# Optimization experiments

Measured on AMD Instinct MI355X. Metric: run time of the kernel, lower is better.

Reference implementation:

```python
import jax, jax.numpy as jnp
import numpy as np

HIDDEN = 1024
HEADS = 16
HEAD_DIM = HIDDEN // HEADS
ROTARY_PCT = 0.25
ROTARY_DIM = int(HEAD_DIM * ROTARY_PCT)  # 16
BASE = 10000.0
SCALE = HEAD_DIM ** -0.5
EPS = 1e-8


def _rotate_half(x):
    h = x.shape[-1] // 2
    return jnp.concatenate([-x[..., h:], x[..., :h]], axis=-1)


def _apply_rope(q, k, position_ids):
    # q, k: [B, H, S, D]; NeoX-style partial rotary on first ROTARY_DIM dims
    inv_freq = 1.0 / (BASE ** (jnp.arange(0, ROTARY_DIM, 2, dtype=jnp.float32) / ROTARY_DIM))
    freqs = position_ids.astype(jnp.float32)[:, None] * inv_freq[None, :]  # [S, rd/2]
    emb = jnp.concatenate([freqs, freqs], axis=-1)  # [S, rd]
    cos = jnp.cos(emb)[None, None, :, :]
    sin = jnp.sin(emb)[None, None, :, :]

    def rot(x):
        x_rot, x_pass = x[..., :ROTARY_DIM], x[..., ROTARY_DIM:]
        x_rot = x_rot * cos + _rotate_half(x_rot) * sin
        return jnp.concatenate([x_rot, x_pass], axis=-1)

    return rot(q), rot(k)


def _ka_scan(attn_weights, value):
    # attn_weights: [B, H, S, S] causal softmax; value: [B, H, S, D]
    # A[0] = V[0]; A[i] = renorm(attn_weights[i, :i]) @ A[:i]
    S = value.shape[2]
    idx = jnp.arange(S)

    def step(a_buf, i):
        w = attn_weights[:, :, i, :]                      # [B, H, S]
        w = jnp.where(idx[None, None, :] < i, w, 0.0)     # strict past only
        w = w / (jnp.sum(w, axis=-1, keepdims=True) + EPS)
        a_i = jnp.einsum('bhs,bhsd->bhd', w, a_buf)
        a_i = jnp.where(i == 0, value[:, :, 0, :], a_i)
        a_buf = jax.lax.dynamic_update_slice(a_buf, a_i[:, :, None, :], (0, 0, i, 0))
        return a_buf, None

    a_buf, _ = jax.lax.scan(step, jnp.zeros_like(value), jnp.arange(S))
    return a_buf


def setup_inputs() -> dict:
    key = jax.random.key(0)
    k1, k2, k3 = jax.random.split(key, 3)
    B, S = 2, 2048
    hidden_states = jax.random.normal(k1, (B, S, HIDDEN), dtype=jnp.float32)
    position_ids = jnp.arange(S, dtype=jnp.int32)
    Wqkv = jax.random.normal(k2, (HIDDEN, 3 * HIDDEN), dtype=jnp.float32) / np.sqrt(HIDDEN)
    bqkv = jnp.zeros((3 * HIDDEN,), dtype=jnp.float32)
    Wd = jax.random.normal(k3, (HIDDEN, HIDDEN), dtype=jnp.float32) / np.sqrt(HIDDEN)
    bd = jnp.zeros((HIDDEN,), dtype=jnp.float32)
    return {"hidden_states": hidden_states, "position_ids": position_ids,
            "Wqkv": Wqkv, "bqkv": bqkv, "Wd": Wd, "bd": bd}


def reference(hidden_states, position_ids, Wqkv, bqkv, Wd, bd):
    B, S, _ = hidden_states.shape
    qkv = hidden_states @ Wqkv + bqkv                       # [B, S, 3*hidden]
    qkv = qkv.reshape(B, S, 3, HEADS, HEAD_DIM).transpose(2, 0, 3, 1, 4)
    query, key, value = qkv[0], qkv[1], qkv[2]              # [B, H, S, D]
    query, key = _apply_rope(query, key, position_ids)

    scores = jnp.einsum('bhqd,bhkd->bhqk', query, key) * SCALE
    causal = jnp.tril(jnp.ones((S, S), dtype=bool))
    scores = jnp.where(causal[None, None], scores, -jnp.inf)
    attn_weights = jax.nn.softmax(scores, axis=-1)          # [B, H, S, S]

    attn_output = _ka_scan(attn_weights, value)             # [B, H, S, D]
    attn_output = attn_output.transpose(0, 2, 1, 3).reshape(B, S, HIDDEN)
    return attn_output @ Wd + bd
```

## Files before the change

### kernel.cpp

```cpp
#include <hip/hip_runtime.h>

#define S_ 2048
#define EPSF 1e-8f
#define SCALEF 0.125f

typedef short bf16x8 __attribute__((ext_vector_type(8)));
typedef float f32x4 __attribute__((ext_vector_type(4)));

__device__ __forceinline__ unsigned short f2bf(float f){
  unsigned int u = __float_as_uint(f);
  u = (u + 0x7fffu + ((u >> 16) & 1u)) >> 16;
  return (unsigned short)u;
}
__device__ __forceinline__ float bf2f(unsigned short h){
  return __uint_as_float(((unsigned int)h) << 16);
}
__device__ __forceinline__ unsigned short f2bf_trunc(float f){
  return (unsigned short)(__float_as_uint(f) >> 16);
}

#define GLD16(g, l) __builtin_amdgcn_global_load_lds( \
    (const __attribute__((address_space(1))) unsigned int*)(g), \
    (__attribute__((address_space(3))) unsigned int*)(l), 16, 0, 0)

__global__ void k_prep(const float* __restrict__ hs, const float* __restrict__ Wqkv,
                       const float* __restrict__ bqkv, const float* __restrict__ Wd,
                       unsigned short* __restrict__ Ab,
                       unsigned short* __restrict__ WT,
                       float* __restrict__ U,
                       float* __restrict__ c_c){
  __shared__ float t[32][33];
  __shared__ float red[4][64];
  __shared__ float vsh[64];
  int bid = blockIdx.x;
  if (bid < 4096){
    int i = (bid * 256 + threadIdx.x) * 4;
    float4 v = *(const float4*)(hs + i);
    ushort4 o; o.x=f2bf(v.x); o.y=f2bf(v.y); o.z=f2bf(v.z); o.w=f2bf(v.w);
    *(ushort4*)(Ab + i) = o;
  } else if (bid < 6144){
    int q = bid - 4096;
    int nt = q & 63, kt = q >> 6;
    int tx = threadIdx.x & 31, ty = threadIdx.x >> 5;
    #pragma unroll
    for (int r = 0; r < 32; r += 8)
      t[ty + r][tx] = Wqkv[(size_t)(kt*32 + ty + r)*3072 + nt*32 + tx];
    __syncthreads();
    #pragma unroll
    for (int r = 0; r < 32; r += 8)
      WT[(size_t)(nt*32 + ty + r)*1024 + kt*32 + tx] = f2bf(t[tx][ty + r]);
  } else if (bid < 6176){
    int bh = bid - 6144; int b = bh >> 4, h = bh & 15;
    int d = threadIdx.x & 63, kc = threadIdx.x >> 6;
    const float* x = hs + (size_t)b * S_ * 1024;
    int col = 2048 + h*64 + d;
    float acc = 0.f;
    #pragma unroll 8
    for (int k = kc*256; k < kc*256 + 256; ++k)
      acc = fmaf(x[k], Wqkv[(size_t)k*3072 + col], acc);
    red[kc][d] = acc;
    __syncthreads();
    if (kc == 0)
      vsh[d] = red[0][d] + red[1][d] + red[2][d] + red[3][d] + bqkv[col];
    __syncthreads();
    for (int n = threadIdx.x; n < 1024; n += 256){
      float a2 = 0.f;
      #pragma unroll 8
      for (int dd = 0; dd < 64; ++dd)
        a2 = fmaf(vsh[dd], Wd[(size_t)(h*64 + dd)*1024 + n], a2);
      U[(size_t)bh*1024 + n] = a2;
    }
  } else {
    int q = bid - 6176;
    float4 z = (float4){0.f,0.f,0.f,0.f};
    *(float4*)(c_c + (size_t)q*1024 + threadIdx.x*4) = z;
  }
}

#define BK 32
__launch_bounds__(256)
__global__ void k_gemm_qk(const unsigned short* __restrict__ Ab,
                          const unsigned short* __restrict__ WT,
                          const float* __restrict__ bqkv,
                          const int* __restrict__ pos_ids,
                          unsigned short* __restrict__ Qb,
                          unsigned short* __restrict__ Kb){
  __shared__ unsigned short At[128*BK];
  __shared__ unsigned short Bt[128*BK];
  const int m0 = blockIdx.y * 128, n0 = blockIdx.x * 128;
  const int w = threadIdx.x >> 6, l = threadIdx.x & 63;
  const int wr = w >> 1, wc = w & 1;
  const int lq = l & 15, lh = l >> 4;
  f32x4 acc[4][4];
  #pragma unroll
  for (int i = 0; i < 4; ++i)
    #pragma unroll
    for (int j = 0; j < 4; ++j) acc[i][j] = (f32x4){0.f,0.f,0.f,0.f};

  const int srow = l >> 2;
  const int scol = (l & 3) * 8;

  for (int kt = 0; kt < 1024; kt += BK){
    GLD16(Ab + (size_t)(m0 + w*32 +      srow)*1024 + kt + scol, &At[(w*32)*BK]);
    GLD16(Ab + (size_t)(m0 + w*32 + 16 + srow)*1024 + kt + scol, &At[(w*32+16)*BK]);
    GLD16(WT + (size_t)(n0 + w*32 +      srow)*1024 + kt + scol, &Bt[(w*32)*BK]);
    GLD16(WT + (size_t)(n0 + w*32 + 16 + srow)*1024 + kt + scol, &Bt[(w*32+16)*BK]);
    __syncthreads();
    bf16x8 af[4], bf[4];
    #pragma unroll
    for (int i = 0; i < 4; ++i)
      af[i] = *(const bf16x8*)&At[(wr*64 + i*16 + lq)*BK + lh*8];
    #pragma unroll
    for (int j = 0; j < 4; ++j)
      bf[j] = *(const bf16x8*)&Bt[(wc*64 + j*16 + lq)*BK + lh*8];
    #pragma unroll
    for (int i = 0; i < 4; ++i)
      #pragma unroll
      for (int j = 0; j < 4; ++j)
        acc[i][j] = __builtin_amdgcn_mfma_f32_16x16x32_bf16(af[i], bf[j], acc[i][j], 0, 0, 0);
    __syncthreads();
  }
  #pragma unroll
  for (int i = 0; i < 4; ++i){
    #pragma unroll
    for (int j = 0; j < 4; ++j){
      #pragma unroll
      for (int r = 0; r < 4; ++r){
        int m = m0 + wr*64 + i*16 + (l>>4)*4 + r;
        int n = n0 + wc*64 + j*16 + (l&15);
        float v = acc[i][j][r] + bqkv[n];
        if (j == 0){
          float partner = __shfl_xor(v, 8);
          int s = m & 2047;
          float pos = (float)pos_ids[s];
          float fr = exp2f(-1.6609640474436813f * (float)(l & 7));
          float th = pos * fr;
          float sn = __sinf(th), cn = __cosf(th);
          v = ((l & 8) == 0) ? (v*cn - partner*sn) : (v*cn + partner*sn);
        }
        int b = m >> 11, s2 = m & 2047;
        int tsel = n >> 10; int nq = n & 1023;
        int h = nq >> 6, d = nq & 63;
        unsigned short* dst = tsel ? Kb : Qb;
        dst[((size_t)(b*16 + h)*S_ + s2)*64 + d] = f2bf(v);
      }
    }
  }
}

#define KST2 66
#define EST 68
__launch_bounds__(256, 4)
__global__ void k_scores(const unsigned short* __restrict__ Qb,
                         const unsigned short* __restrict__ Kb,
                         unsigned short* __restrict__ Eg,
                         float* __restrict__ rinvg){
  __shared__ unsigned short Ks[2][64*KST2];
  __shared__ unsigned short Es[4][16*EST];
  __shared__ float dsh[4][16];
  const int bi = blockIdx.x >> 5, bh = blockIdx.x & 31;
  const unsigned short* Qh = Qb + (size_t)bh * S_ * 64;
  const unsigned short* Kh = Kb + (size_t)bh * S_ * 64;
  const int tid = threadIdx.x, w = tid >> 6, l = tid & 63;
  const int lq = l & 15, lh = l >> 4;
  const unsigned short* qp = Qh + (size_t)(bi*64 + w*16 + lq)*64 + lh*8;
  bf16x8 qf0 = *(const bf16x8*)(qp);
  bf16x8 qf1 = *(const bf16x8*)(qp + 32);
  float dacc[4] = {0.f,0.f,0.f,0.f};
  unsigned short* Etile0 = Eg + ((size_t)bh*528 + (size_t)(bi*(bi+1)/2))*4096;
  const int srow = tid >> 2, sc = (tid & 3)*16;

  {
    const unsigned short* src = Kh + (size_t)srow*64 + sc;
    *(int4*)&Ks[0][srow*KST2 + sc]     = *(const int4*)(src);
    *(int4*)&Ks[0][srow*KST2 + sc + 8] = *(const int4*)(src + 8);
  }
  __syncthreads();

  for (int bj = 0; bj <= bi; ++bj){
    const int cur = bj & 1;
    int4 nk0, nk1;
    if (bj < bi){
      const unsigned short* src = Kh + (size_t)((bj+1)*64 + srow)*64 + sc;
      nk0 = *(const int4*)(src);
      nk1 = *(const int4*)(src + 8);
    }
    unsigned short* Et = Etile0 + (size_t)bj*4096 + w*1024;
    const bool diag = (bj == bi);
    #pragma unroll
    for (int ct = 0; ct < 4; ++ct){
      bf16x8 b0 = *(const bf16x8*)&Ks[cur][(ct*16 + lq)*KST2 + lh*8];
      bf16x8 b1 = *(const bf16x8*)&Ks[cur][(ct*16 + lq)*KST2 + 32 + lh*8];
      f32x4 a = (f32x4){0.f,0.f,0.f,0.f};
      a = __builtin_amdgcn_mfma_f32_16x16x32_bf16(qf0, b0, a, 0, 0, 0);
      a = __builtin_amdgcn_mfma_f32_16x16x32_bf16(qf1, b1, a, 0, 0, 0);
      #pragma unroll
      for (int r = 0; r < 4; ++r){
        float e = __expf(a[r] * SCALEF);
        unsigned short eb = f2bf_trunc(e);
        int rrow = lh*4 + r, col = ct*16 + lq;
        Es[w][rrow*EST + col] = eb;
        float ev = bf2f(eb);
        int grow = w*16 + rrow;
        if (!diag || col < grow) dacc[r] += ev;
        if (diag && col == grow) dsh[w][rrow] = ev;
      }
    }
    #pragma unroll
    for (int it = 0; it < 2; ++it){
      int row = it*8 + (l >> 3), eo = (l & 7)*8;
      *(int4*)(Et + row*64 + eo) = *(const int4*)&Es[w][row*EST + eo];
    }
    if (bj < bi){
      *(int4*)&Ks[cur^1][srow*KST2 + sc]     = nk0;
      *(int4*)&Ks[cur^1][srow*KST2 + sc + 8] = nk1;
    }
    __syncthreads();
  }
  #pragma unroll
  for (int r = 0; r < 4; ++r){
    float d = dacc[r];
    #pragma unroll
    for (int mm = 1; mm < 16; mm <<= 1) d += __shfl_xor(d, mm);
    float dE = dsh[w][lh*4 + r];
    float den = fmaf(EPSF, d + dE, d);
    float rv = 1.0f / den;
    if (lq == 0)
      rinvg[(size_t)bh*S_ + bi*64 + w*16 + lh*4 + r] = rv;
  }
}

__global__ __launch_bounds__(64)
void k_dinv(const unsigned short* __restrict__ Eg,
            const float* __restrict__ rinvg,
            unsigned short* __restrict__ Dg){
  __shared__ float As[64*65];
  const int bh = blockIdx.x >> 5, bi = blockIdx.x & 31;
  const unsigned short* Et =
      Eg + ((size_t)bh*528 + (size_t)(bi*(bi+1)/2) + bi)*4096;
  const int c = threadIdx.x;
  for (int r = 0; r < 64; ++r){
    float rv = rinvg[(size_t)bh*S_ + bi*64 + r];
    float e = bf2f(Et[(r>>4)*1024 + (r&15)*64 + c]);
    As[r*65 + c] = (c < r) ? e * rv : 0.f;
  }
  __syncthreads();
  float X[64];
  #pragma unroll
  for (int r = 0; r < 64; ++r){
    float acc = (r == c) ? 1.f : 0.f;
    #pragma unroll
    for (int k = 0; k < r; ++k)
      acc = fmaf(As[r*65 + k], X[k], acc);
    X[r] = acc;
  }
  unsigned short* dt = Dg + (size_t)blockIdx.x * 4096;
  #pragma unroll
  for (int r = 0; r < 64; ++r)
    dt[(r>>4)*1024 + (r&15)*64 + c] = f2bf(X[r]);
}

__global__ __launch_bounds__(512)
__attribute__((amdgpu_waves_per_eu(2, 2)))
void k_recur3(const unsigned short* __restrict__ Eg,
              const unsigned short* __restrict__ Dg,
              const float* __restrict__ rinvg,
              float* __restrict__ c_c,
              float* __restrict__ c_g){
  __shared__ float Pa[256];
  __shared__ float rso[256];
  __shared__ float csl[2][64];
  __shared__ float bb[64];
  const int bh = blockIdx.x & 31, s = blockIdx.x >> 5;
  const unsigned short* Eh = Eg + (size_t)bh * 528 * 4096;
  const int tid = threadIdx.x, w = tid >> 6, l = tid & 63;
  const int lq = l & 15, lh = l >> 4;

  if (tid < 256){
    Pa[tid] = 0.f;
    rso[tid] = rinvg[(size_t)bh*S_ + (s + 8*(tid >> 6))*64 + l];
  }
  __syncthreads();

  bf16x8 dv0[4], dv1[4];
  if (w == 0){
    const unsigned short* dt = Dg + (size_t)(bh*32 + s)*4096;
    #pragma unroll
    for (int q = 0; q < 4; ++q){
      dv0[q] = *(const bf16x8*)(dt + q*1024 + lq*64 + lh*8);
      dv1[q] = *(const bf16x8*)(dt + q*1024 + lq*64 + 32 + lh*8);
    }
  }

  bf16x8 dA0[3], dA1[3], dB0[3], dB1[3];
  bf16x8 ug0, ug1;
  const int lastc = s + 24;

  auto load_def = [&](int BJ, bf16x8 (&D0)[3], bf16x8 (&D1)[3]){
    int o0 = (BJ >= s) ? (((BJ - s) >> 3) + 1) : 0;
    int ex = (((BJ + 1) & 7) == s) ? 1 : 0;
    int nd = (4 - o0 - ex) * 4;
    if (w >= 1){
      #pragma unroll
      for (int k = 0; k < 3; ++k){
        int t = (w - 1) + k*7;
        if (t < nd){
          int ob = o0 + ex + (t >> 2);
          int bi = s + 8*ob;
          const unsigned short* tp =
              Eh + ((size_t)(bi*(bi+1)/2) + BJ)*4096 + (size_t)(t & 3)*1024;
          D0[k] = *(const bf16x8*)(tp + lq*64 + lh*8);
          D1[k] = *(const bf16x8*)(tp + lq*64 + 32 + lh*8);
        }
      }
      if (ex && w <= 4){
        int bi = BJ + 1;
        const unsigned short* tp =
            Eh + ((size_t)(bi*(bi+1)/2) + BJ)*4096 + (size_t)(w-1)*1024;
        ug0 = *(const bf16x8*)(tp + lq*64 + lh*8);
        ug1 = *(const bf16x8*)(tp + lq*64 + 32 + lh*8);
      }
    }
  };

  auto fold_def = [&](int BJP, bf16x8 (&D0)[3], bf16x8 (&D1)[3], int buf){
    int o0 = (BJP >= s) ? (((BJP - s) >> 3) + 1) : 0;
    int ex = (((BJP + 1) & 7) == s) ? 1 : 0;
    int nd = (4 - o0 - ex) * 4;
    if (w >= 1 && nd > 0){
      bf16x8 dc0 = (bf16x8){0,0,0,0,0,0,0,0};
      bf16x8 dc1 = (bf16x8){0,0,0,0,0,0,0,0};
      if (lq == 0){
        #pragma unroll
        for (int e = 0; e < 8; ++e){
          dc0[e] = (short)f2bf(csl[buf][lh*8 + e]);
          dc1[e] = (short)f2bf(csl[buf][32 + lh*8 + e]);
        }
      }
      #pragma unroll
      for (int k = 0; k < 3; ++k){
        int t = (w - 1) + k*7;
        if (t < nd){
          f32x4 o = (f32x4){0.f,0.f,0.f,0.f};
          o = __builtin_amdgcn_mfma_f32_16x16x32_bf16(D0[k], dc0, o, 0, 0, 0);
          o = __builtin_amdgcn_mfma_f32_16x16x32_bf16(D1[k], dc1, o, 0, 0, 0);
          if (lq == 0){
            int ob = o0 + ex + (t >> 2);
            float* base = Pa + ob*64 + (t & 3)*16 + lh*4;
            float4 v = *(float4*)base;
            v.x += o[0]; v.y += o[1]; v.z += o[2]; v.w += o[3];
            *(float4*)base = v;
          }
        }
      }
    }
  };

  auto iter = [&](int BJ, bf16x8 (&DL0)[3], bf16x8 (&DL1)[3],
                          bf16x8 (&DF0)[3], bf16x8 (&DF1)[3]){
    const int cur = BJ & 1;
    load_def(BJ, DL0, DL1);
    const int ex = (((BJ + 1) & 7) == s) ? 1 : 0;
    if (w == 0){
      if ((BJ & 7) == s){
        const int o = (BJ - s) >> 3;
        float bval = rso[o*64 + l] * Pa[o*64 + l];
        if (BJ == 0 && l == 0) bval = 1.0f;
        bb[l] = bval;
        bf16x8 uc0 = (bf16x8){0,0,0,0,0,0,0,0};
        bf16x8 uc1 = (bf16x8){0,0,0,0,0,0,0,0};
        if (lq == 0){
          #pragma unroll
          for (int e = 0; e < 8; ++e){
            uc0[e] = (short)f2bf(bb[lh*8 + e]);
            uc1[e] = (short)f2bf(bb[32 + lh*8 + e]);
          }
        }
        #pragma unroll
        for (int q = 0; q < 4; ++q){
          f32x4 o4 = (f32x4){0.f,0.f,0.f,0.f};
          o4 = __builtin_amdgcn_mfma_f32_16x16x32_bf16(dv0[q], uc0, o4, 0, 0, 0);
          o4 = __builtin_amdgcn_mfma_f32_16x16x32_bf16(dv1[q], uc1, o4, 0, 0, 0);
          if (lq == 0){
            #pragma unroll
            for (int r = 0; r < 4; ++r)
              csl[cur][q*16 + lh*4 + r] = o4[r];
          }
        }
        float cval = csl[cur][l];
        __hip_atomic_store((unsigned*)(c_c + (size_t)bh*S_ + BJ*64 + l),
                           __float_as_uint(cval),
                           __ATOMIC_RELAXED, __HIP_MEMORY_SCOPE_AGENT);
        c_g[((size_t)(bh >> 4)*S_ + (BJ*64 + l))*16 + (bh & 15)] = cval;
        int bn = BJ + 8;
        if (bn <= lastc){
          const unsigned short* dt = Dg + (size_t)(bh*32 + bn)*4096;
          #pragma unroll
          for (int q = 0; q < 4; ++q){
            dv0[q] = *(const bf16x8*)(dt + q*1024 + lq*64 + lh*8);
            dv1[q] = *(const bf16x8*)(dt + q*1024 + lq*64 + 32 + lh*8);
          }
        }
      } else {
        const unsigned* pp = (const unsigned*)(c_c + (size_t)bh*S_ + BJ*64 + l);
        unsigned v = __hip_atomic_load(pp, __ATOMIC_RELAXED,
                                       __HIP_MEMORY_SCOPE_AGENT);
        while (!__all(v != 0u)){
          __builtin_amdgcn_s_sleep(2);
          v = __hip_atomic_load(pp, __ATOMIC_RELAXED,
                                __HIP_MEMORY_SCOPE_AGENT);
        }
        csl[cur][l] = __uint_as_float(v);
      }
    } else if (BJ >= 1){
      fold_def(BJ - 1, DF0, DF1, cur ^ 1);
    }
    __syncthreads();
    if (ex && w >= 1 && w <= 4){
      bf16x8 uc0 = (bf16x8){0,0,0,0,0,0,0,0};
      bf16x8 uc1 = (bf16x8){0,0,0,0,0,0,0,0};
      if (lq == 0){
        #pragma unroll
        for (int e = 0; e < 8; ++e){
          uc0[e] = (short)f2bf(csl[cur][lh*8 + e]);
          uc1[e] = (short)f2bf(csl[cur][32 + lh*8 + e]);
        }
      }
      f32x4 o = (f32x4){0.f,0.f,0.f,0.f};
      o = __builtin_amdgcn_mfma_f32_16x16x32_bf16(ug0, uc0, o, 0, 0, 0);
      o = __builtin_amdgcn_mfma_f32_16x16x32_bf16(ug1, uc1, o, 0, 0, 0);
      if (lq == 0){
        int ou = (BJ + 1 - s) >> 3;
        float* base = Pa + ou*64 + (w-1)*16 + lh*4;
        float4 v = *(float4*)base;
        v.x += o[0]; v.y += o[1]; v.z += o[2]; v.w += o[3];
        *(float4*)base = v;
      }
    }
    __syncthreads();
  };

  for (int bj = 0; bj <= lastc; bj += 2){
    iter(bj,     dA0, dA1, dB0, dB1);
    if (bj + 1 <= lastc)
      iter(bj+1, dB0, dB1, dA0, dA1);
  }
}

__global__ void k_out(const float* __restrict__ c_g, const float* __restrict__ U,
                      const float* __restrict__ bd, float* __restrict__ out){
  int bs = blockIdx.x; int b = bs >> 11;
  __shared__ float ch[16];
  if (threadIdx.x < 16) ch[threadIdx.x] = c_g[(size_t)bs*16 + threadIdx.x];
  __syncthreads();
  int n = threadIdx.x * 4;
  float4 acc = *(const float4*)(bd + n);
  #pragma unroll
  for (int h = 0; h < 16; ++h){
    float cc = ch[h];
    float4 u = *(const float4*)(U + ((size_t)(b*16 + h))*1024 + n);
    acc.x = fmaf(cc, u.x, acc.x); acc.y = fmaf(cc, u.y, acc.y);
    acc.z = fmaf(cc, u.z, acc.z); acc.w = fmaf(cc, u.w, acc.w);
  }
  *(float4*)(out + (size_t)bs*1024 + n) = acc;
}

extern "C" void kernel_launch(void* const* d_in, const int* in_sizes, int n_in,
                              void* d_out, int out_size, void* d_ws, size_t ws_size,
                              hipStream_t stream) {
  const float* hs   = (const float*)d_in[0];
  const int*   pos  = (const int*)d_in[1];
  const float* Wqkv = (const float*)d_in[2];
  const float* bqkv = (const float*)d_in[3];
  const float* Wd   = (const float*)d_in[4];
  const float* bd   = (const float*)d_in[5];
  float* out = (float*)d_out;

  char* ws = (char*)d_ws;
  unsigned short* Ab = (unsigned short*)(ws);
  unsigned short* Dg = (unsigned short*)(ws);
  unsigned short* WT = (unsigned short*)(ws + (8u<<20));
  unsigned short* Qb = (unsigned short*)(ws + (12u<<20));
  unsigned short* Kb = (unsigned short*)(ws + (20u<<20));
  float* c_g  = (float*)(ws + (28u<<20) + 0x10000);
  float* U    = (float*)(ws + (28u<<20) + 0x50000);
  float* rinvg= (float*)(ws + (28u<<20) + 0x80000);
  float* c_c  = (float*)(ws + (28u<<20) + 0xC0000);
  unsigned short* Eg = (unsigned short*)(ws + (29u<<20));

  k_prep   <<<6240, 256, 0, stream>>>(hs, Wqkv, bqkv, Wd, Ab, WT, U, c_c);
  k_gemm_qk<<<dim3(16, 32), 256, 0, stream>>>(Ab, WT, bqkv, pos, Qb, Kb);
  k_scores <<<1024, 256, 0, stream>>>(Qb, Kb, Eg, rinvg);
  k_dinv   <<<1024, 64, 0, stream>>>(Eg, rinvg, Dg);
  k_recur3 <<<256, 512, 0, stream>>>(Eg, Dg, rinvg, c_c, c_g);
  k_out    <<<4096, 256, 0, stream>>>(c_g, U, bd, out);
}
```

Baseline: 183.3 us.

## Fuse diagonal-block inverse into scores kernel and pair row-blocks for balance

```diff
diff --git a/kernel.cpp b/kernel.cpp
--- a/kernel.cpp
+++ b/kernel.cpp
@@ -154,110 +154,118 @@
 __global__ void k_scores(const unsigned short* __restrict__ Qb,
                          const unsigned short* __restrict__ Kb,
                          unsigned short* __restrict__ Eg,
-                         float* __restrict__ rinvg){
-  __shared__ unsigned short Ks[2][64*KST2];
+                         float* __restrict__ rinvg,
+                         unsigned short* __restrict__ Dg){
+  __shared__ unsigned short Ks[2][64*KST2] __attribute__((aligned(16)));
   __shared__ unsigned short Es[4][16*EST];
   __shared__ float dsh[4][16];
-  const int bi = blockIdx.x >> 5, bh = blockIdx.x & 31;
+  __shared__ float rvs[64];
+  float* As = (float*)&Ks[0][0];
+  const int p = blockIdx.x >> 5, bh = blockIdx.x & 31;
   const unsigned short* Qh = Qb + (size_t)bh * S_ * 64;
   const unsigned short* Kh = Kb + (size_t)bh * S_ * 64;
   const int tid = threadIdx.x, w = tid >> 6, l = tid & 63;
   const int lq = l & 15, lh = l >> 4;
-  const unsigned short* qp = Qh + (size_t)(bi*64 + w*16 + lq)*64 + lh*8;
-  bf16x8 qf0 = *(const bf16x8*)(qp);
-  bf16x8 qf1 = *(const bf16x8*)(qp + 32);
-  float dacc[4] = {0.f,0.f,0.f,0.f};
-  unsigned short* Etile0 = Eg + ((size_t)bh*528 + (size_t)(bi*(bi+1)/2))*4096;
   const int srow = tid >> 2, sc = (tid & 3)*16;
 
-  {
-    const unsigned short* src = Kh + (size_t)srow*64 + sc;
-    *(int4*)&Ks[0][srow*KST2 + sc]     = *(const int4*)(src);
-    *(int4*)&Ks[0][srow*KST2 + sc + 8] = *(const int4*)(src + 8);
-  }
-  __syncthreads();
-
-  for (int bj = 0; bj <= bi; ++bj){
-    const int cur = bj & 1;
-    int4 nk0, nk1;
-    if (bj < bi){
-      const unsigned short* src = Kh + (size_t)((bj+1)*64 + srow)*64 + sc;
-      nk0 = *(const int4*)(src);
-      nk1 = *(const int4*)(src + 8);
-    }
-    unsigned short* Et = Etile0 + (size_t)bj*4096 + w*1024;
-    const bool diag = (bj == bi);
-    #pragma unroll
-    for (int ct = 0; ct < 4; ++ct){
-      bf16x8 b0 = *(const bf16x8*)&Ks[cur][(ct*16 + lq)*KST2 + lh*8];
-      bf16x8 b1 = *(const bf16x8*)&Ks[cur][(ct*16 + lq)*KST2 + 32 + lh*8];
-      f32x4 a = (f32x4){0.f,0.f,0.f,0.f};
-      a = __builtin_amdgcn_mfma_f32_16x16x32_bf16(qf0, b0, a, 0, 0, 0);
-      a = __builtin_amdgcn_mfma_f32_16x16x32_bf16(qf1, b1, a, 0, 0, 0);
-      #pragma unroll
-      for (int r = 0; r < 4; ++r){
-        float e = __expf(a[r] * SCALEF);
-        unsigned short eb = f2bf_trunc(e);
-        int rrow = lh*4 + r, col = ct*16 + lq;
-        Es[w][rrow*EST + col] = eb;
-        float ev = bf2f(eb);
-        int grow = w*16 + rrow;
-        if (!diag || col < grow) dacc[r] += ev;
-        if (diag && col == grow) dsh[w][rrow] = ev;
-      }
-    }
-    #pragma unroll
-    for (int it = 0; it < 2; ++it){
-      int row = it*8 + (l >> 3), eo = (l & 7)*8;
-      *(int4*)(Et + row*64 + eo) = *(const int4*)&Es[w][row*EST + eo];
-    }
-    if (bj < bi){
-      *(int4*)&Ks[cur^1][srow*KST2 + sc]     = nk0;
-      *(int4*)&Ks[cur^1][srow*KST2 + sc + 8] = nk1;
-    }
-    __syncthreads();
-  }
-  #pragma unroll
-  for (int r = 0; r < 4; ++r){
-    float d = dacc[r];
-    #pragma unroll
-    for (int mm = 1; mm < 16; mm <<= 1) d += __shfl_xor(d, mm);
-    float dE = dsh[w][lh*4 + r];
-    float den = fmaf(EPSF, d + dE, d);
-    float rv = 1.0f / den;
-    if (lq == 0)
-      rinvg[(size_t)bh*S_ + bi*64 + w*16 + lh*4 + r] = rv;
-  }
-}
-
-__global__ __launch_bounds__(64)
-void k_dinv(const unsigned short* __restrict__ Eg,
-            const float* __restrict__ rinvg,
-            unsigned short* __restrict__ Dg){
-  __shared__ float As[64*65];
-  const int bh = blockIdx.x >> 5, bi = blockIdx.x & 31;
-  const unsigned short* Et =
-      Eg + ((size_t)bh*528 + (size_t)(bi*(bi+1)/2) + bi)*4096;
-  const int c = threadIdx.x;
-  for (int r = 0; r < 64; ++r){
-    float rv = rinvg[(size_t)bh*S_ + bi*64 + r];
-    float e = bf2f(Et[(r>>4)*1024 + (r&15)*64 + c]);
-    As[r*65 + c] = (c < r) ? e * rv : 0.f;
-  }
-  __syncthreads();
-  float X[64];
-  #pragma unroll
-  for (int r = 0; r < 64; ++r){
-    float acc = (r == c) ? 1.f : 0.f;
-    #pragma unroll
-    for (int k = 0; k < r; ++k)
-      acc = fmaf(As[r*65 + k], X[k], acc);
-    X[r] = acc;
-  }
-  unsigned short* dt = Dg + (size_t)blockIdx.x * 4096;
-  #pragma unroll
-  for (int r = 0; r < 64; ++r)
-    dt[(r>>4)*1024 + (r&15)*64 + c] = f2bf(X[r]);
+  for (int ph = 0; ph < 2; ++ph){
+    const int bi = ph ? (31 - p) : p;
+    const unsigned short* qp = Qh + (size_t)(bi*64 + w*16 + lq)*64 + lh*8;
+    bf16x8 qf0 = *(const bf16x8*)(qp);
+    bf16x8 qf1 = *(const bf16x8*)(qp + 32);
+    float dacc[4] = {0.f,0.f,0.f,0.f};
+    unsigned short* Etile0 = Eg + ((size_t)bh*528 + (size_t)(bi*(bi+1)/2))*4096;
+
+    {
+      const unsigned short* src = Kh + (size_t)srow*64 + sc;
+      *(int4*)&Ks[0][srow*KST2 + sc]     = *(const int4*)(src);
+      *(int4*)&Ks[0][srow*KST2 + sc + 8] = *(const int4*)(src + 8);
+    }
+    __syncthreads();
+
+    for (int bj = 0; bj <= bi; ++bj){
+      const int cur = bj & 1;
+      int4 nk0, nk1;
+      if (bj < bi){
+        const unsigned short* src = Kh + (size_t)((bj+1)*64 + srow)*64 + sc;
+        nk0 = *(const int4*)(src);
+        nk1 = *(const int4*)(src + 8);
+      }
+      unsigned short* Et = Etile0 + (size_t)bj*4096 + w*1024;
+      const bool diag = (bj == bi);
+      #pragma unroll
+      for (int ct = 0; ct < 4; ++ct){
+        bf16x8 b0 = *(const bf16x8*)&Ks[cur][(ct*16 + lq)*KST2 + lh*8];
+        bf16x8 b1 = *(const bf16x8*)&Ks[cur][(ct*16 + lq)*KST2 + 32 + lh*8];
+        f32x4 a = (f32x4){0.f,0.f,0.f,0.f};
+        a = __builtin_amdgcn_mfma_f32_16x16x32_bf16(qf0, b0, a, 0, 0, 0);
+        a = __builtin_amdgcn_mfma_f32_16x16x32_bf16(qf1, b1, a, 0, 0, 0);
+        #pragma unroll
+        for (int r = 0; r < 4; ++r){
+          float e = __expf(a[r] * SCALEF);
+          unsigned short eb = f2bf_trunc(e);
+          int rrow = lh*4 + r, col = ct*16 + lq;
+          Es[w][rrow*EST + col] = eb;
+          float ev = bf2f(eb);
+          int grow = w*16 + rrow;
+          if (!diag || col < grow) dacc[r] += ev;
+          if (diag && col == grow) dsh[w][rrow] = ev;
+        }
+      }
+      #pragma unroll
+      for (int it = 0; it < 2; ++it){
+        int row = it*8 + (l >> 3), eo = (l & 7)*8;
+        *(int4*)(Et + row*64 + eo) = *(const int4*)&Es[w][row*EST + eo];
+      }
+      if (bj < bi){
+        *(int4*)&Ks[cur^1][srow*KST2 + sc]     = nk0;
+        *(int4*)&Ks[cur^1][srow*KST2 + sc + 8] = nk1;
+      }
+      __syncthreads();
+    }
+    #pragma unroll
+    for (int r = 0; r < 4; ++r){
+      float d = dacc[r];
+      #pragma unroll
+      for (int mm = 1; mm < 16; mm <<= 1) d += __shfl_xor(d, mm);
+      float dE = dsh[w][lh*4 + r];
+      float den = fmaf(EPSF, d + dE, d);
+      float rv = 1.0f / den;
+      if (lq == 0){
+        rinvg[(size_t)bh*S_ + bi*64 + w*16 + lh*4 + r] = rv;
+        rvs[w*16 + lh*4 + r] = rv;
+      }
+    }
+    __syncthreads();
+    {
+      int r = tid >> 2, c0 = (tid & 3)*16;
+      float rv = rvs[r];
+      #pragma unroll
+      for (int cc = 0; cc < 16; ++cc){
+        int c = c0 + cc;
+        float e = bf2f(Es[r >> 4][(r & 15)*EST + c]);
+        As[r*65 + c] = (c < r) ? e * rv : 0.f;
+      }
+    }
+    __syncthreads();
+    if (w == 0){
+      const int c = l;
+      float X[64];
+      #pragma unroll
+      for (int r = 0; r < 64; ++r){
+        float acc = (r == c) ? 1.f : 0.f;
+        #pragma unroll
+        for (int k = 0; k < r; ++k)
+          acc = fmaf(As[r*65 + k], X[k], acc);
+        X[r] = acc;
+      }
+      unsigned short* dt = Dg + (size_t)(bh*32 + bi) * 4096;
+      #pragma unroll
+      for (int r = 0; r < 64; ++r)
+        dt[(r>>4)*1024 + (r&15)*64 + c] = f2bf(X[r]);
+    }
+    __syncthreads();
+  }
 }
 
 __global__ __launch_bounds__(512)
@@ -490,8 +498,7 @@
 
   k_prep   <<<6240, 256, 0, stream>>>(hs, Wqkv, bqkv, Wd, Ab, WT, U, c_c);
   k_gemm_qk<<<dim3(16, 32), 256, 0, stream>>>(Ab, WT, bqkv, pos, Qb, Kb);
-  k_scores <<<1024, 256, 0, stream>>>(Qb, Kb, Eg, rinvg);
-  k_dinv   <<<1024, 64, 0, stream>>>(Eg, rinvg, Dg);
+  k_scores <<<512, 256, 0, stream>>>(Qb, Kb, Eg, rinvg, Dg);
   k_recur3 <<<256, 512, 0, stream>>>(Eg, Dg, rinvg, c_c, c_g);
   k_out    <<<4096, 256, 0, stream>>>(c_g, U, bd, out);
 }
```

Measured after the change: 236.5 us. 1.29x slower.
